# Kernel optimization log

Hardware: AMD Instinct MI355X
Metric: run time of the kernel (lower is better)

Reference implementation:

```python
import jax, jax.numpy as jnp
import numpy as np

# Object condensation loss config (matches init_kwargs / HGCalML defaults)
Q_MIN = 0.5
S_B = 1.0
POT_SCALE = 1.0
REP_SCALE = 1.0
BETA_SCALE = 1.0
E_WEIGHT = 1.0
HUBER_DELTA = 2.0
E_DEN_OFFSET = 1.0
K_MAX = 192          # object-id slots per event; id 0 = noise
EPS = 1e-6

B, N = 4, 50000


def setup_inputs() -> dict:
    key = jax.random.key(0)
    k1, k2, k3, k4, k5 = jax.random.split(key, 5)
    return {
        "beta": jax.random.uniform(k1, (B, N, 1), dtype=jnp.float32),
        "ccoords": jax.random.normal(k2, (B, N, 2), dtype=jnp.float32),
        "pred_energy": jax.random.uniform(k3, (B, N, 1), dtype=jnp.float32),
        "true_energy": jax.random.uniform(k4, (B, N, 1), dtype=jnp.float32),
        "truth_idx": jax.random.randint(k5, (B, N), 0, K_MAX, dtype=jnp.int32),
    }


def _per_event(beta, ccoords, pred_e, true_e, tidx):
    # beta: [N,1], ccoords: [N,2], tidx: [N] int (0 = noise)
    beta = jnp.clip(beta[:, 0], 1e-4, 1.0 - 1e-4)            # [N]
    q = jnp.arctanh(beta) ** 2 + Q_MIN                        # charge  [N]

    ids = jnp.arange(K_MAX)
    M = (tidx[:, None] == ids[None, :]) & (ids[None, :] > 0)  # [N,K] membership
    Mf = M.astype(q.dtype)
    obj_valid = jnp.any(M, axis=0)                            # [K]
    vf = obj_valid.astype(q.dtype)

    # condensation point alpha_k = argmax_q over members of object k
    qM = jnp.where(M, q[:, None], -1.0)                       # [N,K]
    idx_alpha = jnp.argmax(qM, axis=0)                        # [K]
    x_alpha = ccoords[idx_alpha]                              # [K,2]
    q_alpha = q[idx_alpha]                                    # [K]
    beta_alpha = beta[idx_alpha]                              # [K]

    # pairwise hit<->condensation-point distances
    d2 = jnp.sum((ccoords[:, None, :] - x_alpha[None, :, :]) ** 2, axis=-1)  # [N,K]

    # attractive potential (members), repulsive hinge (non-members of valid objects)
    att = jnp.sum(d2 * q_alpha[None, :] * Mf, axis=-1)                       # [N]
    dist = jnp.sqrt(d2 + EPS)
    rep = jnp.sum(jnp.maximum(0.0, 1.0 - dist) * q_alpha[None, :]
                  * (1.0 - Mf) * vf[None, :], axis=-1)                       # [N]
    L_V = jnp.mean(q * (POT_SCALE * att + REP_SCALE * rep))

    n_obj = jnp.sum(vf) + EPS
    L_beta = BETA_SCALE * jnp.sum((1.0 - beta_alpha) * vf) / n_obj

    noise = (tidx == 0).astype(q.dtype)
    L_noise = S_B * jnp.sum(beta * noise) / (jnp.sum(noise) + EPS)

    # energy payload loss: relative error, Huber, beta-weighted per object
    ediff = (pred_e[:, 0] - true_e[:, 0]) / (true_e[:, 0] + E_DEN_OFFSET)
    ad = jnp.abs(ediff)
    eh = jnp.where(ad <= HUBER_DELTA, 0.5 * ad ** 2,
                   HUBER_DELTA * (ad - 0.5 * HUBER_DELTA))                   # [N]
    pw = Mf * beta[:, None]                                                  # [N,K]
    per_obj_e = jnp.sum(pw * eh[:, None], axis=0) / (jnp.sum(pw, axis=0) + EPS)
    L_E = E_WEIGHT * jnp.sum(per_obj_e * vf) / n_obj

    return L_V + L_beta + L_noise + L_E


def reference(beta, ccoords, pred_energy, true_energy, truth_idx):
    per_ev = jax.vmap(_per_event)(beta, ccoords, pred_energy, true_energy, truth_idx)
    return jnp.mean(per_ev)
```

## Files before the change

### kernel.cpp

```cpp
#include <hip/hip_runtime.h>
#include <math.h>

#define KM 192
#define EPSF 1e-6f
#define QMIN 0.5f
#define BLK 256
#define HA 4
#define TILEA (BLK * HA)

__device__ __forceinline__ float clipb(float b) {
    return fminf(fmaxf(b, 1e-4f), 1.0f - 1e-4f);
}
__device__ __forceinline__ float fast_atanh(float b) {
    float r = (1.f + b) * __builtin_amdgcn_rcpf(1.f - b);
    return 0.34657359f * __builtin_amdgcn_logf(r);
}
__device__ __forceinline__ float bcast(float v, int j) {
    return __int_as_float(__builtin_amdgcn_readlane(__float_as_int(v), j));
}

__global__ void __launch_bounds__(BLK)
k_pre(const float* __restrict__ beta, const int* __restrict__ tidx,
      const float* __restrict__ pe,   const float* __restrict__ te,
      unsigned long long* __restrict__ packs,
      float* __restrict__ enm, float* __restrict__ eden,
      float* __restrict__ scal, int N) {
    const int e = blockIdx.y;
    __shared__ unsigned long long smax[KM];
    __shared__ float sn[KM], sd[KM];
    __shared__ float sw[8];
    if (threadIdx.x < KM) { smax[threadIdx.x] = 0ull; sn[threadIdx.x] = 0.f; sd[threadIdx.x] = 0.f; }
    __syncthreads();

    const size_t base = (size_t)e * N;
    float bn = 0.f, cn = 0.f;
    #pragma unroll
    for (int h = 0; h < HA; ++h) {
        int i = blockIdx.x * TILEA + h * BLK + threadIdx.x;
        if (i < N) {
            int   t  = tidx[base + i];
            float bc = clipb(beta[base + i]);
            if (t > 0) {
                unsigned long long pack =
                    ((unsigned long long)__float_as_uint(bc) << 32) |
                    (unsigned long long)(unsigned)(N - 1 - i);
                atomicMax(&smax[t], pack);
                float tev = te[base + i];
                float edv = (pe[base + i] - tev) * __builtin_amdgcn_rcpf(tev + 1.f);
                float ad  = fabsf(edv);
                float eh  = (ad <= 2.f) ? 0.5f * ad * ad : 2.f * (ad - 1.f);
                atomicAdd(&sn[t], bc * eh);
                atomicAdd(&sd[t], bc);
            } else { bn += bc; cn += 1.f; }
        }
    }
    __syncthreads();

    if (threadIdx.x < KM) {
        unsigned long long v = smax[threadIdx.x];
        if (v) atomicMax(&packs[e * KM + threadIdx.x], v);
        float vd = sd[threadIdx.x];
        if (vd != 0.f) {
            atomicAdd(&enm [e * KM + threadIdx.x], sn[threadIdx.x]);
            atomicAdd(&eden[e * KM + threadIdx.x], vd);
        }
    }
    for (int off = 32; off > 0; off >>= 1) {
        bn += __shfl_down(bn, off);
        cn += __shfl_down(cn, off);
    }
    const int wid = threadIdx.x >> 6;
    if ((threadIdx.x & 63) == 0) { sw[wid] = bn; sw[4 + wid] = cn; }
    __syncthreads();
    if (threadIdx.x == 0) {
        atomicAdd(&scal[e * 8 + 3], (sw[0] + sw[1]) + (sw[2] + sw[3]));
        atomicAdd(&scal[e * 8 + 4], (sw[4] + sw[5]) + (sw[6] + sw[7]));
    }
}

__global__ void __launch_bounds__(BLK, 4)
k_main(const float* __restrict__ beta, const float* __restrict__ cc,
       const int* __restrict__ tidx,
       const unsigned long long* __restrict__ packs,
       float* __restrict__ abw,
       const float* __restrict__ enm, const float* __restrict__ eden,
       float* __restrict__ scal, unsigned int* __restrict__ cnt,
       float* __restrict__ out, int N, int B) {
    const int e = blockIdx.y;
    __shared__ float4 sa[KM];
    __shared__ float  sw[12];
    __shared__ int    lastFlag;

    if (threadIdx.x < KM) {
        unsigned long long v = packs[e * KM + threadIdx.x];
        float4 a = make_float4(0.f, 0.f, 0.f, 0.f);
        if (v) {
            int idx  = N - 1 - (int)(unsigned)(v & 0xffffffffull);
            float bw = __uint_as_float((unsigned)(v >> 32));
            float at = fast_atanh(bw);
            float2 cp = ((const float2*)cc)[(size_t)e * N + idx];
            a = make_float4(cp.x, cp.y, fmaf(at, at, QMIN), bw);
        }
        sa[threadIdx.x] = a;
        if (blockIdx.x == 0) abw[e * KM + threadIdx.x] = a.w;
    }
    __syncthreads();

    const int lane = threadIdx.x & 63;
    const float4 o0 = sa[lane];
    const float4 o1 = sa[lane + 64];
    const float4 o2 = sa[lane + 128];

    const size_t base = (size_t)e * N;
    const int i = blockIdx.x * BLK + threadIdx.x;
    const bool ok = i < N;
    const size_t ii = base + (ok ? i : 0);
    const float2 cp = ((const float2*)cc)[ii];
    const float  bc = clipb(beta[ii]);
    const int    t  = ok ? tidx[ii] : -1;
    const float  at = fast_atanh(bc);
    const float  qh = ok ? fmaf(at, at, QMIN) : 0.f;

    float lvh = 0.f;
    if (t > 0) {
        float4 av = sa[t];
        float dx = cp.x - av.x, dy = cp.y - av.y;
        float d2 = fmaf(dx, dx, dy * dy);
        float hin = fmaxf(1.f - __builtin_amdgcn_sqrtf(d2 + EPSF), 0.f);
        lvh = qh * av.z * (d2 - hin);
    }

    float r0 = 0.f, r1 = 0.f, r2 = 0.f;
    #pragma unroll 16
    for (int j = 0; j < 64; ++j) {
        const float xh = bcast(cp.x, j);
        const float yh = bcast(cp.y, j);
        const float qb = bcast(qh,  j);
        float dx0 = o0.x - xh, dy0 = o0.y - yh;
        float dx1 = o1.x - xh, dy1 = o1.y - yh;
        float dx2 = o2.x - xh, dy2 = o2.y - yh;
        float d0 = fmaf(dx0, dx0, fmaf(dy0, dy0, EPSF));
        float d1 = fmaf(dx1, dx1, fmaf(dy1, dy1, EPSF));
        float d2 = fmaf(dx2, dx2, fmaf(dy2, dy2, EPSF));
        r0 = fmaf(fmaxf(1.f - __builtin_amdgcn_sqrtf(d0), 0.f), qb, r0);
        r1 = fmaf(fmaxf(1.f - __builtin_amdgcn_sqrtf(d1), 0.f), qb, r1);
        r2 = fmaf(fmaxf(1.f - __builtin_amdgcn_sqrtf(d2), 0.f), qb, r2);
    }
    float lv = fmaf(o0.z, r0, fmaf(o1.z, r1, fmaf(o2.z, r2, lvh)));
    __syncthreads();

    for (int off = 32; off > 0; off >>= 1) lv += __shfl_down(lv, off);
    const int wid = threadIdx.x >> 6;
    if ((threadIdx.x & 63) == 0) sw[wid] = lv;
    __syncthreads();
    if (threadIdx.x == 0)
        atomicAdd(&scal[e * 8 + 0], (sw[0] + sw[1]) + (sw[2] + sw[3]));

    if (threadIdx.x == 0) {
        __threadfence();
        unsigned int old = atomicAdd(&cnt[0], 1u);
        lastFlag = (old == gridDim.x * gridDim.y - 1u);
    }
    __syncthreads();
    if (!lastFlag) return;
    __threadfence();

    volatile float* vab = abw;
    volatile float* vsc = scal;
    float tot = 0.f;
    for (int ev = 0; ev < B; ++ev) {
        float lb = 0.f, nv = 0.f, le = 0.f;
        if (threadIdx.x < KM) {
            float bw = vab[ev * KM + threadIdx.x];
            if (bw > 0.f) {
                lb = 1.f - bw;
                nv = 1.f;
                le = enm[ev * KM + threadIdx.x] / (eden[ev * KM + threadIdx.x] + EPSF);
            }
        }
        for (int off = 32; off > 0; off >>= 1) {
            lb += __shfl_down(lb, off);
            nv += __shfl_down(nv, off);
            le += __shfl_down(le, off);
        }
        if ((threadIdx.x & 63) == 0) { sw[wid] = lb; sw[4 + wid] = nv; sw[8 + wid] = le; }
        __syncthreads();
        if (threadIdx.x == 0) {
            float lbs = (sw[0] + sw[1]) + (sw[2] + sw[3]);
            float nvs = (sw[4] + sw[5]) + (sw[6] + sw[7]);
            float les = (sw[8] + sw[9]) + (sw[10] + sw[11]);
            float nobj = nvs + EPSF;
            tot += vsc[ev * 8 + 0] / (float)N + lbs / nobj
                 + vsc[ev * 8 + 3] / (vsc[ev * 8 + 4] + EPSF) + les / nobj;
        }
        __syncthreads();
    }
    if (threadIdx.x == 0) out[0] = tot / (float)B;
}

extern "C" void kernel_launch(void* const* d_in, const int* in_sizes, int n_in,
                              void* d_out, int out_size, void* d_ws, size_t ws_size,
                              hipStream_t stream) {
    const int B = 4;
    const int N = in_sizes[0] / B;
    const int HBT = (N + TILEA - 1) / TILEA;
    const int MB  = (N + BLK - 1) / BLK;

    const float* beta = (const float*)d_in[0];
    const float* cc   = (const float*)d_in[1];
    const float* pe   = (const float*)d_in[2];
    const float* te   = (const float*)d_in[3];
    const int*   tidx = (const int*)  d_in[4];
    float* out = (float*)d_out;

    char* ws = (char*)d_ws;
    unsigned long long* packs = (unsigned long long*)ws;
    float* abw  = (float*)(ws + (size_t)B * KM * 8);
    float* enm  = abw  + B * KM;
    float* eden = enm  + B * KM;
    float* scal = eden + B * KM;
    unsigned int* cnt = (unsigned int*)(scal + B * 8);
    const size_t zeroBytes = (char*)(cnt + 16) - ws;

    (void)hipMemsetAsync(d_ws, 0, zeroBytes, stream);
    k_pre<<<dim3(HBT, B), dim3(BLK), 0, stream>>>(beta, tidx, pe, te, packs, enm, eden, scal, N);
    k_main<<<dim3(MB, B), dim3(BLK), 0, stream>>>(
        beta, cc, tidx, packs, abw, enm, eden, scal, cnt, out, N, B);
}
```

Before: 95.27 us.

## Fuse pre-pass and main pass into one persistent kernel with grid barrier

Merges the two kernels into a single persistent kernel of 256 blocks (64 tiles per event, 512 threads). The blocks grid-stride over the hits and meet at a spin-wait grid barrier on an atomic counter between the condensation-point pass and the repulsion pass. This removes one kernel launch and the gap between launches, and drops the abw buffer by reading packs directly in the final reduction. The cost is that every block must be resident at once or the barrier deadlocks, and each block now loops over several hit chunks, which reduces parallelism.

Result: slower. 113.8 us (+19.5%).

```diff
diff --git a/kernel.cpp b/kernel.cpp
--- a/kernel.cpp
+++ b/kernel.cpp
@@ -4,9 +4,8 @@
 #define KM 192
 #define EPSF 1e-6f
 #define QMIN 0.5f
-#define BLK 256
-#define HA 4
-#define TILEA (BLK * HA)
+#define BT 512
+#define TPE 64
 
 __device__ __forceinline__ float clipb(float b) {
     return fminf(fmaxf(b, 1e-4f), 1.0f - 1e-4f);
@@ -18,25 +17,42 @@
 __device__ __forceinline__ float bcast(float v, int j) {
     return __int_as_float(__builtin_amdgcn_readlane(__float_as_int(v), j));
 }
-
-__global__ void __launch_bounds__(BLK)
-k_pre(const float* __restrict__ beta, const int* __restrict__ tidx,
-      const float* __restrict__ pe,   const float* __restrict__ te,
-      unsigned long long* __restrict__ packs,
-      float* __restrict__ enm, float* __restrict__ eden,
-      float* __restrict__ scal, int N) {
-    const int e = blockIdx.y;
+__device__ __forceinline__ unsigned long long aload64(const unsigned long long* p) {
+    return __hip_atomic_load(p, __ATOMIC_RELAXED, __HIP_MEMORY_SCOPE_AGENT);
+}
+__device__ __forceinline__ float aloadf(const float* p) {
+    return __hip_atomic_load(p, __ATOMIC_RELAXED, __HIP_MEMORY_SCOPE_AGENT);
+}
+
+__global__ void __launch_bounds__(BT, 2)
+k_fused(const float* __restrict__ beta, const float* __restrict__ cc,
+        const float* __restrict__ pe,   const float* __restrict__ te,
+        const int* __restrict__ tidx,
+        unsigned long long* __restrict__ packs,
+        float* __restrict__ enm, float* __restrict__ eden,
+        float* __restrict__ scal, unsigned int* __restrict__ cnt,
+        float* __restrict__ out, int N) {
+    const int e    = blockIdx.x & 3;
+    const int tile = blockIdx.x >> 2;
+    const int tid  = threadIdx.x;
+    const int lane = tid & 63;
+    const int wv   = tid >> 6;
+    const int NBLK = gridDim.x;
+    const size_t base = (size_t)e * N;
+    const int STRIDE = TPE * BT;
+
     __shared__ unsigned long long smax[KM];
     __shared__ float sn[KM], sd[KM];
-    __shared__ float sw[8];
-    if (threadIdx.x < KM) { smax[threadIdx.x] = 0ull; sn[threadIdx.x] = 0.f; sd[threadIdx.x] = 0.f; }
-    __syncthreads();
-
-    const size_t base = (size_t)e * N;
+    __shared__ float4 sa[KM];
+    __shared__ float sw[24];
+    __shared__ int lastFlag;
+
+    if (tid < KM) { smax[tid] = 0ull; sn[tid] = 0.f; sd[tid] = 0.f; }
+    __syncthreads();
+
     float bn = 0.f, cn = 0.f;
-    #pragma unroll
-    for (int h = 0; h < HA; ++h) {
-        int i = blockIdx.x * TILEA + h * BLK + threadIdx.x;
+    for (int s = 0; tile * BT + s * STRIDE < N; ++s) {
+        int i = tile * BT + s * STRIDE + tid;
         if (i < N) {
             int   t  = tidx[base + i];
             float bc = clipb(beta[base + i]);
@@ -55,127 +71,120 @@
         }
     }
     __syncthreads();
-
-    if (threadIdx.x < KM) {
-        unsigned long long v = smax[threadIdx.x];
-        if (v) atomicMax(&packs[e * KM + threadIdx.x], v);
-        float vd = sd[threadIdx.x];
+    if (tid < KM) {
+        unsigned long long v = smax[tid];
+        if (v) atomicMax(&packs[e * KM + tid], v);
+        float vd = sd[tid];
         if (vd != 0.f) {
-            atomicAdd(&enm [e * KM + threadIdx.x], sn[threadIdx.x]);
-            atomicAdd(&eden[e * KM + threadIdx.x], vd);
+            atomicAdd(&enm [e * KM + tid], sn[tid]);
+            atomicAdd(&eden[e * KM + tid], vd);
         }
     }
     for (int off = 32; off > 0; off >>= 1) {
         bn += __shfl_down(bn, off);
         cn += __shfl_down(cn, off);
     }
-    const int wid = threadIdx.x >> 6;
-    if ((threadIdx.x & 63) == 0) { sw[wid] = bn; sw[4 + wid] = cn; }
-    __syncthreads();
-    if (threadIdx.x == 0) {
-        atomicAdd(&scal[e * 8 + 3], (sw[0] + sw[1]) + (sw[2] + sw[3]));
-        atomicAdd(&scal[e * 8 + 4], (sw[4] + sw[5]) + (sw[6] + sw[7]));
-    }
-}
-
-__global__ void __launch_bounds__(BLK, 4)
-k_main(const float* __restrict__ beta, const float* __restrict__ cc,
-       const int* __restrict__ tidx,
-       const unsigned long long* __restrict__ packs,
-       float* __restrict__ abw,
-       const float* __restrict__ enm, const float* __restrict__ eden,
-       float* __restrict__ scal, unsigned int* __restrict__ cnt,
-       float* __restrict__ out, int N, int B) {
-    const int e = blockIdx.y;
-    __shared__ float4 sa[KM];
-    __shared__ float  sw[12];
-    __shared__ int    lastFlag;
-
-    if (threadIdx.x < KM) {
-        unsigned long long v = packs[e * KM + threadIdx.x];
+    if (lane == 0) { sw[wv] = bn; sw[8 + wv] = cn; }
+    __syncthreads();
+    if (tid == 0) {
+        float b2 = 0.f, c2 = 0.f;
+        #pragma unroll
+        for (int w = 0; w < 8; ++w) { b2 += sw[w]; c2 += sw[8 + w]; }
+        atomicAdd(&scal[e * 8 + 3], b2);
+        atomicAdd(&scal[e * 8 + 4], c2);
+    }
+
+    if (tid == 0) {
+        __threadfence();
+        __hip_atomic_fetch_add(&cnt[0], 1u, __ATOMIC_ACQ_REL, __HIP_MEMORY_SCOPE_AGENT);
+        while (__hip_atomic_load(&cnt[0], __ATOMIC_ACQUIRE, __HIP_MEMORY_SCOPE_AGENT)
+               < (unsigned)NBLK) { __builtin_amdgcn_s_sleep(1); }
+    }
+    __syncthreads();
+
+    if (tid < KM) {
+        unsigned long long v = aload64(&packs[e * KM + tid]);
         float4 a = make_float4(0.f, 0.f, 0.f, 0.f);
         if (v) {
             int idx  = N - 1 - (int)(unsigned)(v & 0xffffffffull);
             float bw = __uint_as_float((unsigned)(v >> 32));
             float at = fast_atanh(bw);
-            float2 cp = ((const float2*)cc)[(size_t)e * N + idx];
+            float2 cp = ((const float2*)cc)[base + idx];
             a = make_float4(cp.x, cp.y, fmaf(at, at, QMIN), bw);
         }
-        sa[threadIdx.x] = a;
-        if (blockIdx.x == 0) abw[e * KM + threadIdx.x] = a.w;
-    }
-    __syncthreads();
-
-    const int lane = threadIdx.x & 63;
+        sa[tid] = a;
+    }
+    __syncthreads();
+
     const float4 o0 = sa[lane];
     const float4 o1 = sa[lane + 64];
     const float4 o2 = sa[lane + 128];
 
-    const size_t base = (size_t)e * N;
-    const int i = blockIdx.x * BLK + threadIdx.x;
-    const bool ok = i < N;
-    const size_t ii = base + (ok ? i : 0);
-    const float2 cp = ((const float2*)cc)[ii];
-    const float  bc = clipb(beta[ii]);
-    const int    t  = ok ? tidx[ii] : -1;
-    const float  at = fast_atanh(bc);
-    const float  qh = ok ? fmaf(at, at, QMIN) : 0.f;
-
-    float lvh = 0.f;
-    if (t > 0) {
-        float4 av = sa[t];
-        float dx = cp.x - av.x, dy = cp.y - av.y;
-        float d2 = fmaf(dx, dx, dy * dy);
-        float hin = fmaxf(1.f - __builtin_amdgcn_sqrtf(d2 + EPSF), 0.f);
-        lvh = qh * av.z * (d2 - hin);
-    }
-
-    float r0 = 0.f, r1 = 0.f, r2 = 0.f;
-    #pragma unroll 16
-    for (int j = 0; j < 64; ++j) {
-        const float xh = bcast(cp.x, j);
-        const float yh = bcast(cp.y, j);
-        const float qb = bcast(qh,  j);
-        float dx0 = o0.x - xh, dy0 = o0.y - yh;
-        float dx1 = o1.x - xh, dy1 = o1.y - yh;
-        float dx2 = o2.x - xh, dy2 = o2.y - yh;
-        float d0 = fmaf(dx0, dx0, fmaf(dy0, dy0, EPSF));
-        float d1 = fmaf(dx1, dx1, fmaf(dy1, dy1, EPSF));
-        float d2 = fmaf(dx2, dx2, fmaf(dy2, dy2, EPSF));
-        r0 = fmaf(fmaxf(1.f - __builtin_amdgcn_sqrtf(d0), 0.f), qb, r0);
-        r1 = fmaf(fmaxf(1.f - __builtin_amdgcn_sqrtf(d1), 0.f), qb, r1);
-        r2 = fmaf(fmaxf(1.f - __builtin_amdgcn_sqrtf(d2), 0.f), qb, r2);
+    float r0 = 0.f, r1 = 0.f, r2 = 0.f, lvh = 0.f;
+    for (int s = 0; tile * BT + wv * 64 + s * STRIDE < N; ++s) {
+        const int i = tile * BT + wv * 64 + s * STRIDE + lane;
+        const bool ok = i < N;
+        const size_t ii = base + (ok ? i : 0);
+        const float2 cp = ((const float2*)cc)[ii];
+        const float  bc = clipb(beta[ii]);
+        const int    t  = ok ? tidx[ii] : 0;
+        const float  at = fast_atanh(bc);
+        const float  qh = ok ? fmaf(at, at, QMIN) : 0.f;
+
+        if (t > 0) {
+            float4 av = sa[t];
+            float dx = cp.x - av.x, dy = cp.y - av.y;
+            float d2 = fmaf(dx, dx, dy * dy);
+            float hin = fmaxf(1.f - __builtin_amdgcn_sqrtf(d2 + EPSF), 0.f);
+            lvh = fmaf(qh * av.z, d2 - hin, lvh);
+        }
+        #pragma unroll 16
+        for (int j = 0; j < 64; ++j) {
+            const float xh = bcast(cp.x, j);
+            const float yh = bcast(cp.y, j);
+            const float qb = bcast(qh,  j);
+            float dx0 = o0.x - xh, dy0 = o0.y - yh;
+            float dx1 = o1.x - xh, dy1 = o1.y - yh;
+            float dx2 = o2.x - xh, dy2 = o2.y - yh;
+            float d0 = fmaf(dx0, dx0, fmaf(dy0, dy0, EPSF));
+            float d1 = fmaf(dx1, dx1, fmaf(dy1, dy1, EPSF));
+            float d2 = fmaf(dx2, dx2, fmaf(dy2, dy2, EPSF));
+            r0 = fmaf(fmaxf(1.f - __builtin_amdgcn_sqrtf(d0), 0.f), qb, r0);
+            r1 = fmaf(fmaxf(1.f - __builtin_amdgcn_sqrtf(d1), 0.f), qb, r1);
+            r2 = fmaf(fmaxf(1.f - __builtin_amdgcn_sqrtf(d2), 0.f), qb, r2);
+        }
     }
     float lv = fmaf(o0.z, r0, fmaf(o1.z, r1, fmaf(o2.z, r2, lvh)));
-    __syncthreads();
-
     for (int off = 32; off > 0; off >>= 1) lv += __shfl_down(lv, off);
-    const int wid = threadIdx.x >> 6;
-    if ((threadIdx.x & 63) == 0) sw[wid] = lv;
-    __syncthreads();
-    if (threadIdx.x == 0)
-        atomicAdd(&scal[e * 8 + 0], (sw[0] + sw[1]) + (sw[2] + sw[3]));
-
-    if (threadIdx.x == 0) {
+    if (lane == 0) sw[wv] = lv;
+    __syncthreads();
+    if (tid == 0) {
+        float a = 0.f;
+        #pragma unroll
+        for (int w = 0; w < 8; ++w) a += sw[w];
+        atomicAdd(&scal[e * 8 + 0], a);
+    }
+
+    if (tid == 0) {
         __threadfence();
-        unsigned int old = atomicAdd(&cnt[0], 1u);
-        lastFlag = (old == gridDim.x * gridDim.y - 1u);
+        unsigned int old = __hip_atomic_fetch_add(&cnt[1], 1u, __ATOMIC_ACQ_REL,
+                                                  __HIP_MEMORY_SCOPE_AGENT);
+        lastFlag = (old == (unsigned)NBLK - 1u);
     }
     __syncthreads();
     if (!lastFlag) return;
     __threadfence();
 
-    volatile float* vab = abw;
-    volatile float* vsc = scal;
     float tot = 0.f;
-    for (int ev = 0; ev < B; ++ev) {
+    for (int ev = 0; ev < 4; ++ev) {
         float lb = 0.f, nv = 0.f, le = 0.f;
-        if (threadIdx.x < KM) {
-            float bw = vab[ev * KM + threadIdx.x];
-            if (bw > 0.f) {
-                lb = 1.f - bw;
+        if (tid < KM) {
+            unsigned long long v = aload64(&packs[ev * KM + tid]);
+            if (v) {
+                lb = 1.f - __uint_as_float((unsigned)(v >> 32));
                 nv = 1.f;
-                le = enm[ev * KM + threadIdx.x] / (eden[ev * KM + threadIdx.x] + EPSF);
+                le = aloadf(&enm[ev * KM + tid]) /
+                     (aloadf(&eden[ev * KM + tid]) + EPSF);
             }
         }
         for (int off = 32; off > 0; off >>= 1) {
@@ -183,19 +192,20 @@
             nv += __shfl_down(nv, off);
             le += __shfl_down(le, off);
         }
-        if ((threadIdx.x & 63) == 0) { sw[wid] = lb; sw[4 + wid] = nv; sw[8 + wid] = le; }
+        if (lane == 0) { sw[wv] = lb; sw[8 + wv] = nv; sw[16 + wv] = le; }
         __syncthreads();
-        if (threadIdx.x == 0) {
-            float lbs = (sw[0] + sw[1]) + (sw[2] + sw[3]);
-            float nvs = (sw[4] + sw[5]) + (sw[6] + sw[7]);
-            float les = (sw[8] + sw[9]) + (sw[10] + sw[11]);
+        if (tid == 0) {
+            float lbs = 0.f, nvs = 0.f, les = 0.f;
+            #pragma unroll
+            for (int w = 0; w < 8; ++w) { lbs += sw[w]; nvs += sw[8 + w]; les += sw[16 + w]; }
             float nobj = nvs + EPSF;
-            tot += vsc[ev * 8 + 0] / (float)N + lbs / nobj
-                 + vsc[ev * 8 + 3] / (vsc[ev * 8 + 4] + EPSF) + les / nobj;
+            tot += aloadf(&scal[ev * 8 + 0]) / (float)N + lbs / nobj
+                 + aloadf(&scal[ev * 8 + 3]) / (aloadf(&scal[ev * 8 + 4]) + EPSF)
+                 + les / nobj;
         }
         __syncthreads();
     }
-    if (threadIdx.x == 0) out[0] = tot / (float)B;
+    if (tid == 0) out[0] = tot * 0.25f;
 }
 
 extern "C" void kernel_launch(void* const* d_in, const int* in_sizes, int n_in,
@@ -203,8 +213,6 @@
                               hipStream_t stream) {
     const int B = 4;
     const int N = in_sizes[0] / B;
-    const int HBT = (N + TILEA - 1) / TILEA;
-    const int MB  = (N + BLK - 1) / BLK;
 
     const float* beta = (const float*)d_in[0];
     const float* cc   = (const float*)d_in[1];
@@ -215,15 +223,13 @@
 
     char* ws = (char*)d_ws;
     unsigned long long* packs = (unsigned long long*)ws;
-    float* abw  = (float*)(ws + (size_t)B * KM * 8);
-    float* enm  = abw  + B * KM;
+    float* enm  = (float*)(ws + (size_t)B * KM * 8);
     float* eden = enm  + B * KM;
     float* scal = eden + B * KM;
     unsigned int* cnt = (unsigned int*)(scal + B * 8);
     const size_t zeroBytes = (char*)(cnt + 16) - ws;
 
     (void)hipMemsetAsync(d_ws, 0, zeroBytes, stream);
-    k_pre<<<dim3(HBT, B), dim3(BLK), 0, stream>>>(beta, tidx, pe, te, packs, enm, eden, scal, N);
-    k_main<<<dim3(MB, B), dim3(BLK), 0, stream>>>(
-        beta, cc, tidx, packs, abw, enm, eden, scal, cnt, out, N, B);
-}
+    k_fused<<<dim3(TPE * B), dim3(BT), 0, stream>>>(
+        beta, cc, pe, te, tidx, packs, enm, eden, scal, cnt, out, N);
+}
```

## Replace global atomics and memset with per-tile partials and a reduction kernel

Applied to the files above, without the earlier changes.

Each pre-pass block now writes its per-object max/sum partials and noise sums to per-tile slots instead of using global atomics. A new per-event reduction kernel combines them, computes the condensation points and the scalar loss terms, and resets the completion counter, so the memset launch goes away. The main kernel writes per-block potential partials and the last block sums them. The unroll factor also drops from 16 to 8 and the launch_bounds occupancy hint is removed. This adds a kernel launch and a small serial reduction over about 49 tiles per event. It also relies on the counter being zero on the very first call, since no memset clears it any more.

Result: slower. 104.5 us (+9.7%).

```diff
diff --git a/kernel.cpp b/kernel.cpp
--- a/kernel.cpp
+++ b/kernel.cpp
@@ -22,21 +22,20 @@
 __global__ void __launch_bounds__(BLK)
 k_pre(const float* __restrict__ beta, const int* __restrict__ tidx,
       const float* __restrict__ pe,   const float* __restrict__ te,
-      unsigned long long* __restrict__ packs,
-      float* __restrict__ enm, float* __restrict__ eden,
-      float* __restrict__ scal, int N) {
-    const int e = blockIdx.y;
+      unsigned long long* __restrict__ pm, float* __restrict__ pn,
+      float* __restrict__ pd, float* __restrict__ pb, int N, int HBT) {
+    const int e = blockIdx.y, tile = blockIdx.x, tid = threadIdx.x;
     __shared__ unsigned long long smax[KM];
     __shared__ float sn[KM], sd[KM];
     __shared__ float sw[8];
-    if (threadIdx.x < KM) { smax[threadIdx.x] = 0ull; sn[threadIdx.x] = 0.f; sd[threadIdx.x] = 0.f; }
+    if (tid < KM) { smax[tid] = 0ull; sn[tid] = 0.f; sd[tid] = 0.f; }
     __syncthreads();
 
     const size_t base = (size_t)e * N;
     float bn = 0.f, cn = 0.f;
     #pragma unroll
     for (int h = 0; h < HA; ++h) {
-        int i = blockIdx.x * TILEA + h * BLK + threadIdx.x;
+        int i = tile * TILEA + h * BLK + tid;
         if (i < N) {
             int   t  = tidx[base + i];
             float bc = clipb(beta[base + i]);
@@ -56,43 +55,42 @@
     }
     __syncthreads();
 
-    if (threadIdx.x < KM) {
-        unsigned long long v = smax[threadIdx.x];
-        if (v) atomicMax(&packs[e * KM + threadIdx.x], v);
-        float vd = sd[threadIdx.x];
-        if (vd != 0.f) {
-            atomicAdd(&enm [e * KM + threadIdx.x], sn[threadIdx.x]);
-            atomicAdd(&eden[e * KM + threadIdx.x], vd);
-        }
+    const size_t row = (size_t)(e * HBT + tile) * KM;
+    if (tid < KM) {
+        pm[row + tid] = smax[tid];
+        pn[row + tid] = sn[tid];
+        pd[row + tid] = sd[tid];
     }
     for (int off = 32; off > 0; off >>= 1) {
         bn += __shfl_down(bn, off);
         cn += __shfl_down(cn, off);
     }
-    const int wid = threadIdx.x >> 6;
-    if ((threadIdx.x & 63) == 0) { sw[wid] = bn; sw[4 + wid] = cn; }
-    __syncthreads();
-    if (threadIdx.x == 0) {
-        atomicAdd(&scal[e * 8 + 3], (sw[0] + sw[1]) + (sw[2] + sw[3]));
-        atomicAdd(&scal[e * 8 + 4], (sw[4] + sw[5]) + (sw[6] + sw[7]));
-    }
-}
-
-__global__ void __launch_bounds__(BLK, 4)
-k_main(const float* __restrict__ beta, const float* __restrict__ cc,
-       const int* __restrict__ tidx,
-       const unsigned long long* __restrict__ packs,
-       float* __restrict__ abw,
-       const float* __restrict__ enm, const float* __restrict__ eden,
-       float* __restrict__ scal, unsigned int* __restrict__ cnt,
-       float* __restrict__ out, int N, int B) {
-    const int e = blockIdx.y;
-    __shared__ float4 sa[KM];
-    __shared__ float  sw[12];
-    __shared__ int    lastFlag;
-
-    if (threadIdx.x < KM) {
-        unsigned long long v = packs[e * KM + threadIdx.x];
+    const int wv = tid >> 6;
+    if ((tid & 63) == 0) { sw[wv] = bn; sw[4 + wv] = cn; }
+    __syncthreads();
+    if (tid == 0) {
+        pb[(size_t)(e * HBT + tile) * 2 + 0] = (sw[0] + sw[1]) + (sw[2] + sw[3]);
+        pb[(size_t)(e * HBT + tile) * 2 + 1] = (sw[4] + sw[5]) + (sw[6] + sw[7]);
+    }
+}
+
+__global__ void __launch_bounds__(BLK)
+k_red(const unsigned long long* __restrict__ pm, const float* __restrict__ pn,
+      const float* __restrict__ pd, const float* __restrict__ pb,
+      const float* __restrict__ cc, float4* __restrict__ alpha,
+      float* __restrict__ cpart, unsigned int* __restrict__ cnt, int N, int HBT) {
+    const int e = blockIdx.x, tid = threadIdx.x;
+    __shared__ float sred[20];
+    float lb = 0.f, nv = 0.f, le = 0.f;
+    if (tid < KM) {
+        unsigned long long v = 0ull;
+        float ns = 0.f, ds = 0.f;
+        for (int t = 0; t < HBT; ++t) {
+            size_t o = (size_t)(e * HBT + t) * KM + tid;
+            unsigned long long p = pm[o];
+            if (p > v) v = p;
+            ns += pn[o]; ds += pd[o];
+        }
         float4 a = make_float4(0.f, 0.f, 0.f, 0.f);
         if (v) {
             int idx  = N - 1 - (int)(unsigned)(v & 0xffffffffull);
@@ -100,24 +98,66 @@
             float at = fast_atanh(bw);
             float2 cp = ((const float2*)cc)[(size_t)e * N + idx];
             a = make_float4(cp.x, cp.y, fmaf(at, at, QMIN), bw);
-        }
-        sa[threadIdx.x] = a;
-        if (blockIdx.x == 0) abw[e * KM + threadIdx.x] = a.w;
-    }
-    __syncthreads();
-
-    const int lane = threadIdx.x & 63;
+            lb = 1.f - bw; nv = 1.f; le = ns / (ds + EPSF);
+        }
+        alpha[e * KM + tid] = a;
+    }
+    float bn = 0.f, cn = 0.f;
+    for (int t = tid; t < HBT; t += BLK) {
+        bn += pb[(size_t)(e * HBT + t) * 2 + 0];
+        cn += pb[(size_t)(e * HBT + t) * 2 + 1];
+    }
+    for (int off = 32; off > 0; off >>= 1) {
+        lb += __shfl_down(lb, off);
+        nv += __shfl_down(nv, off);
+        le += __shfl_down(le, off);
+        bn += __shfl_down(bn, off);
+        cn += __shfl_down(cn, off);
+    }
+    const int wv = tid >> 6;
+    if ((tid & 63) == 0) {
+        sred[wv] = lb; sred[4 + wv] = nv; sred[8 + wv] = le;
+        sred[12 + wv] = bn; sred[16 + wv] = cn;
+    }
+    __syncthreads();
+    if (tid == 0) {
+        float lbs = 0.f, nvs = 0.f, les = 0.f, bns = 0.f, cns = 0.f;
+        #pragma unroll
+        for (int w = 0; w < 4; ++w) {
+            lbs += sred[w]; nvs += sred[4 + w]; les += sred[8 + w];
+            bns += sred[12 + w]; cns += sred[16 + w];
+        }
+        float nobj = nvs + EPSF;
+        cpart[e] = lbs / nobj + bns / (cns + EPSF) + les / nobj;
+        if (e == 0) cnt[0] = 0u;
+    }
+}
+
+__global__ void __launch_bounds__(BLK)
+k_main(const float* __restrict__ beta, const float* __restrict__ cc,
+       const int* __restrict__ tidx,  const float4* __restrict__ alpha,
+       const float* __restrict__ cpart, float* __restrict__ lvp,
+       unsigned int* __restrict__ cnt, float* __restrict__ out,
+       int N, int MB2) {
+    const int e = blockIdx.y, tile = blockIdx.x, tid = threadIdx.x;
+    const int lane = tid & 63, wv = tid >> 6;
+    __shared__ float4 sa[KM];
+    __shared__ float sw[16];
+    __shared__ int lastFlag;
+    if (tid < KM) sa[tid] = alpha[e * KM + tid];
+    __syncthreads();
+
     const float4 o0 = sa[lane];
     const float4 o1 = sa[lane + 64];
     const float4 o2 = sa[lane + 128];
 
     const size_t base = (size_t)e * N;
-    const int i = blockIdx.x * BLK + threadIdx.x;
+    const int i = tile * BLK + wv * 64 + lane;
     const bool ok = i < N;
     const size_t ii = base + (ok ? i : 0);
     const float2 cp = ((const float2*)cc)[ii];
     const float  bc = clipb(beta[ii]);
-    const int    t  = ok ? tidx[ii] : -1;
+    const int    t  = ok ? tidx[ii] : 0;
     const float  at = fast_atanh(bc);
     const float  qh = ok ? fmaf(at, at, QMIN) : 0.f;
 
@@ -131,7 +171,7 @@
     }
 
     float r0 = 0.f, r1 = 0.f, r2 = 0.f;
-    #pragma unroll 16
+    #pragma unroll 8
     for (int j = 0; j < 64; ++j) {
         const float xh = bcast(cp.x, j);
         const float yh = bcast(cp.y, j);
@@ -147,16 +187,14 @@
         r2 = fmaf(fmaxf(1.f - __builtin_amdgcn_sqrtf(d2), 0.f), qb, r2);
     }
     float lv = fmaf(o0.z, r0, fmaf(o1.z, r1, fmaf(o2.z, r2, lvh)));
-    __syncthreads();
 
     for (int off = 32; off > 0; off >>= 1) lv += __shfl_down(lv, off);
-    const int wid = threadIdx.x >> 6;
-    if ((threadIdx.x & 63) == 0) sw[wid] = lv;
-    __syncthreads();
-    if (threadIdx.x == 0)
-        atomicAdd(&scal[e * 8 + 0], (sw[0] + sw[1]) + (sw[2] + sw[3]));
-
-    if (threadIdx.x == 0) {
+    if (lane == 0) sw[wv] = lv;
+    __syncthreads();
+    if (tid == 0)
+        lvp[e * MB2 + tile] = (sw[0] + sw[1]) + (sw[2] + sw[3]);
+
+    if (tid == 0) {
         __threadfence();
         unsigned int old = atomicAdd(&cnt[0], 1u);
         lastFlag = (old == gridDim.x * gridDim.y - 1u);
@@ -165,37 +203,20 @@
     if (!lastFlag) return;
     __threadfence();
 
-    volatile float* vab = abw;
-    volatile float* vsc = scal;
-    float tot = 0.f;
-    for (int ev = 0; ev < B; ++ev) {
-        float lb = 0.f, nv = 0.f, le = 0.f;
-        if (threadIdx.x < KM) {
-            float bw = vab[ev * KM + threadIdx.x];
-            if (bw > 0.f) {
-                lb = 1.f - bw;
-                nv = 1.f;
-                le = enm[ev * KM + threadIdx.x] / (eden[ev * KM + threadIdx.x] + EPSF);
-            }
-        }
-        for (int off = 32; off > 0; off >>= 1) {
-            lb += __shfl_down(lb, off);
-            nv += __shfl_down(nv, off);
-            le += __shfl_down(le, off);
-        }
-        if ((threadIdx.x & 63) == 0) { sw[wid] = lb; sw[4 + wid] = nv; sw[8 + wid] = le; }
-        __syncthreads();
-        if (threadIdx.x == 0) {
-            float lbs = (sw[0] + sw[1]) + (sw[2] + sw[3]);
-            float nvs = (sw[4] + sw[5]) + (sw[6] + sw[7]);
-            float les = (sw[8] + sw[9]) + (sw[10] + sw[11]);
-            float nobj = nvs + EPSF;
-            tot += vsc[ev * 8 + 0] / (float)N + lbs / nobj
-                 + vsc[ev * 8 + 3] / (vsc[ev * 8 + 4] + EPSF) + les / nobj;
-        }
-        __syncthreads();
-    }
-    if (threadIdx.x == 0) out[0] = tot / (float)B;
+    float s = 0.f;
+    for (int idx = tid; idx < 4 * MB2; idx += BLK) s += lvp[idx];
+    float c = (tid < 4) ? cpart[tid] : 0.f;
+    for (int off = 32; off > 0; off >>= 1) {
+        s += __shfl_down(s, off);
+        c += __shfl_down(c, off);
+    }
+    if (lane == 0) { sw[wv] = s; sw[8 + wv] = c; }
+    __syncthreads();
+    if (tid == 0) {
+        float ssum = (sw[0] + sw[1]) + (sw[2] + sw[3]);
+        float csum = (sw[8] + sw[9]) + (sw[10] + sw[11]);
+        out[0] = ssum / (4.f * (float)N) + csum * 0.25f;
+    }
 }
 
 extern "C" void kernel_launch(void* const* d_in, const int* in_sizes, int n_in,
@@ -204,7 +225,7 @@
     const int B = 4;
     const int N = in_sizes[0] / B;
     const int HBT = (N + TILEA - 1) / TILEA;
-    const int MB  = (N + BLK - 1) / BLK;
+    const int MB2 = (N + BLK - 1) / BLK;
 
     const float* beta = (const float*)d_in[0];
     const float* cc   = (const float*)d_in[1];
@@ -214,16 +235,19 @@
     float* out = (float*)d_out;
 
     char* ws = (char*)d_ws;
-    unsigned long long* packs = (unsigned long long*)ws;
-    float* abw  = (float*)(ws + (size_t)B * KM * 8);
-    float* enm  = abw  + B * KM;
-    float* eden = enm  + B * KM;
-    float* scal = eden + B * KM;
-    unsigned int* cnt = (unsigned int*)(scal + B * 8);
-    const size_t zeroBytes = (char*)(cnt + 16) - ws;
-
-    (void)hipMemsetAsync(d_ws, 0, zeroBytes, stream);
-    k_pre<<<dim3(HBT, B), dim3(BLK), 0, stream>>>(beta, tidx, pe, te, packs, enm, eden, scal, N);
-    k_main<<<dim3(MB, B), dim3(BLK), 0, stream>>>(
-        beta, cc, tidx, packs, abw, enm, eden, scal, cnt, out, N, B);
-}
+    unsigned long long* pm = (unsigned long long*)ws;
+    float* pn = (float*)(ws + (size_t)B * HBT * KM * 8);
+    float* pd = pn + (size_t)B * HBT * KM;
+    float* pb = pd + (size_t)B * HBT * KM;
+    size_t off = (size_t)B * HBT * KM * 16 + (size_t)B * HBT * 2 * 4;
+    off = (off + 15) & ~(size_t)15;
+    float4* alpha = (float4*)(ws + off);
+    float* cpart = (float*)(alpha + B * KM);
+    float* lvp   = cpart + 4;
+    unsigned int* cnt = (unsigned int*)(lvp + B * MB2);
+
+    k_pre<<<dim3(HBT, B), dim3(BLK), 0, stream>>>(beta, tidx, pe, te, pm, pn, pd, pb, N, HBT);
+    k_red<<<dim3(B), dim3(BLK), 0, stream>>>(pm, pn, pd, pb, cc, alpha, cpart, cnt, N, HBT);
+    k_main<<<dim3(MB2, B), dim3(BLK), 0, stream>>>(
+        beta, cc, tidx, alpha, cpart, lvp, cnt, out, N, MB2);
+}
```
